# Kernel optimization log

Hardware: AMD Instinct MI355X
Metric: run time of the kernel (lower is better)

The kernel has to match this reference:

```python
import jax, jax.numpy as jnp
import numpy as np

NEG_SLOPE = 0.2


def gat_conv(x, src, dst, n, W, a_src, a_dst, b):
    # x: [N, Din], W: [Din, Dout], a_src/a_dst: [Dout], b: [Dout]
    h = x @ W                                   # [N, Dout]
    alpha_src = h @ a_src                       # [N] score contribution of source nodes
    alpha_dst = h @ a_dst                       # [N]
    e = jax.nn.leaky_relu(alpha_src[src] + alpha_dst[dst], NEG_SLOPE)  # [E]
    # segment softmax over destination nodes (every node has a self-loop -> no empty segs)
    m = jax.ops.segment_max(e, dst, num_segments=n)
    p = jnp.exp(e - m[dst])
    denom = jax.ops.segment_sum(p, dst, num_segments=n)
    coeff = p / denom[dst]                      # [E]
    out = jax.ops.segment_sum(h[src] * coeff[:, None], dst, num_segments=n)
    return out + b


def setup_inputs() -> dict:
    key = jax.random.key(0)
    ks = jax.random.split(key, 16)
    N, E, D_IN, D_H, C = 50000, 800000, 256, 256, 10
    x = jax.random.normal(ks[0], (N, D_IN), dtype=jnp.float32)
    edge_index = jax.random.randint(ks[1], (2, E), 0, N, dtype=jnp.int64)
    s = 0.1
    params = {
        "W1": jax.random.normal(ks[2], (D_IN, D_H), jnp.float32) * s,
        "a_src1": jax.random.normal(ks[3], (D_H,), jnp.float32) * s,
        "a_dst1": jax.random.normal(ks[4], (D_H,), jnp.float32) * s,
        "b1": jnp.zeros((D_H,), jnp.float32),
        "W2": jax.random.normal(ks[5], (D_H, D_H), jnp.float32) * s,
        "a_src2": jax.random.normal(ks[6], (D_H,), jnp.float32) * s,
        "a_dst2": jax.random.normal(ks[7], (D_H,), jnp.float32) * s,
        "b2": jnp.zeros((D_H,), jnp.float32),
        "W3": jax.random.normal(ks[8], (D_H, C), jnp.float32) * s,
        "a_src3": jax.random.normal(ks[9], (C,), jnp.float32) * s,
        "a_dst3": jax.random.normal(ks[10], (C,), jnp.float32) * s,
        "b3": jnp.zeros((C,), jnp.float32),
    }
    return {"x": x, "edge_index": edge_index, **params}


def reference(x, edge_index, W1, a_src1, a_dst1, b1, W2, a_src2, a_dst2, b2,
              W3, a_src3, a_dst3, b3):
    n = x.shape[0]
    # PyG GATConv default add_self_loops=True
    loops = jnp.arange(n, dtype=edge_index.dtype)
    src = jnp.concatenate([edge_index[0], loops])
    dst = jnp.concatenate([edge_index[1], loops])
    h = gat_conv(x, src, dst, n, W1, a_src1, a_dst1, b1)
    h = jax.nn.relu(h)
    h = gat_conv(h, src, dst, n, W2, a_src2, a_dst2, b2)
    h = jax.nn.relu(h)
    out = gat_conv(h, src, dst, n, W3, a_src3, a_dst3, b3)
    return out
```

## Files before the change

kernel.cpp:

```cpp
#include <hip/hip_runtime.h>
#include <math.h>

#define N_NODES 50000
#define N_EDGES 800000
#define EP (N_EDGES + N_NODES)
#define NEG_SLOPE 0.2f
#define SCAN_BLOCKS ((N_NODES + 255) / 256)

typedef short short8 __attribute__((ext_vector_type(8)));
typedef float float4_ __attribute__((ext_vector_type(4)));

__device__ __forceinline__ unsigned short f2bf(float f) {
  unsigned int u = __float_as_uint(f);
  u = (u + 0x7FFFu + ((u >> 16) & 1u)) >> 16;
  return (unsigned short)u;
}
__device__ __forceinline__ float bf2f(unsigned int us) {
  return __uint_as_float(us << 16);
}
__device__ __forceinline__ unsigned int pack2(float lo, float hi) {
  return (unsigned int)f2bf(lo) | ((unsigned int)f2bf(hi) << 16);
}

__device__ __forceinline__ int permc(int p) {
  return ((p & 0xE) << 4) | ((p & 1) << 4) | (p >> 4);
}


template <int PERM>
__global__ void cvt_wf_kernel(const float* __restrict__ W, unsigned short* __restrict__ Wf) {
  int t = blockIdx.x * 256 + threadIdx.x;
  int f = t >> 6, lane = t & 63;
  int nt = f >> 3, k0t = f & 7;
  int lm = lane & 15, kg = lane >> 4;
  int kbase = k0t * 32 + kg * 8;
  int n = nt * 16 + lm;
  short8 v;
#pragma unroll
  for (int j = 0; j < 8; ++j) {
    int k = PERM ? permc(kbase + j) : (kbase + j);
    v[j] = (short)f2bf(W[(size_t)k * 256 + n]);
  }
  ((short8*)Wf)[t] = v;
}

__global__ void cvt_wf3_kernel(const float* __restrict__ W3, unsigned short* __restrict__ Wf3) {
  int t = blockIdx.x * 256 + threadIdx.x;
  int k0t = t >> 6, lane = t & 63;
  int lm = lane & 15, kg = lane >> 4;
  int kbase = k0t * 32 + kg * 8;
  short8 v;
#pragma unroll
  for (int j = 0; j < 8; ++j) {
    int k = permc(kbase + j);
    v[j] = (lm < 10) ? (short)f2bf(W3[(size_t)k * 10 + lm]) : (short)0;
  }
  ((short8*)Wf3)[t] = v;
}

__global__ void permute_bias_kernel(const float* __restrict__ b1, const float* __restrict__ b2,
                                    float* __restrict__ pb1, float* __restrict__ pb2) {
  int p = threadIdx.x;
  int c = permc(p);
  pb1[p] = b1[c];
  pb2[p] = b2[c];
}


__global__ void count_kernel(const int* __restrict__ ei, int* __restrict__ cnt) {
  int e = blockIdx.x * 256 + threadIdx.x;
  if (e >= EP) return;
  int dst = (e < N_EDGES) ? ei[N_EDGES + e] : (e - N_EDGES);
  atomicAdd(&cnt[dst], 1);
}

__global__ void scan1_kernel(const int* __restrict__ cnt, int* __restrict__ off,
                             int* __restrict__ bsum) {
  int i = blockIdx.x * 256 + threadIdx.x;
  int v = (i < N_NODES) ? cnt[i] : 0;
  int lane = threadIdx.x & 63, w = threadIdx.x >> 6;
  int x = v;
  for (int o = 1; o < 64; o <<= 1) { int y = __shfl_up(x, o); if (lane >= o) x += y; }
  __shared__ int wsum[4];
  if (lane == 63) wsum[w] = x;
  __syncthreads();
  int add = 0;
  for (int k = 0; k < w; ++k) add += wsum[k];
  if (i < N_NODES) off[i] = x - v + add;
  if (threadIdx.x == 255) bsum[blockIdx.x] = add + x;
}

__global__ void scan2_kernel(int* __restrict__ bsum, int* __restrict__ bpre,
                             int* __restrict__ off) {
  int t = threadIdx.x;
  int v = (t < SCAN_BLOCKS) ? bsum[t] : 0;
  int lane = t & 63, w = t >> 6;
  int x = v;
  for (int o = 1; o < 64; o <<= 1) { int y = __shfl_up(x, o); if (lane >= o) x += y; }
  __shared__ int wsum[4];
  if (lane == 63) wsum[w] = x;
  __syncthreads();
  int add = 0;
  for (int k = 0; k < w; ++k) add += wsum[k];
  if (t < SCAN_BLOCKS) bpre[t] = x - v + add;
  if (t == 255) off[N_NODES] = add + x;
}

__global__ void scan3_kernel(int* __restrict__ off, const int* __restrict__ bpre) {
  int i = blockIdx.x * 256 + threadIdx.x;
  if (i < N_NODES) off[i] += bpre[blockIdx.x];
}

__global__ void scatter_kernel(const int* __restrict__ ei, const int* __restrict__ off,
                               int* __restrict__ cnt, int* __restrict__ esrc) {
  int e = blockIdx.x * 256 + threadIdx.x;
  if (e >= EP) return;
  int src, dst;
  if (e < N_EDGES) { src = ei[e]; dst = ei[N_EDGES + e]; }
  else { src = dst = e - N_EDGES; }
  int pos = off[dst] + atomicAdd(&cnt[dst], 1);
  esrc[pos] = src;
}


template <int AF32>
__global__ __launch_bounds__(512, 2) void gemm_mfma4(const void* __restrict__ Av,
                                                     const uint4* __restrict__ Wf,
                                                     unsigned short* __restrict__ C,
                                                     const float* __restrict__ asrc,
                                                     const float* __restrict__ adst,
                                                     float* __restrict__ as_,
                                                     float* __restrict__ ad_, int M) {
  __shared__ uint4 Bl[8192];
  int tid = threadIdx.x;
#pragma unroll
  for (int i = 0; i < 16; ++i) Bl[i * 512 + tid] = Wf[i * 512 + tid];
  int wave = tid >> 6, lane = tid & 63;
  int lm = lane & 15, kg = lane >> 4;
  int row0 = blockIdx.x * 256 + wave * 32;
  int ar0 = row0 + lm, ar1 = row0 + 16 + lm;
  if (ar0 >= M) ar0 = M - 1;
  if (ar1 >= M) ar1 = M - 1;

  auto loadA = [&](int k0t, int ar) -> short8 {
    if (AF32) {
      const float* A = (const float*)Av;
      const float* p = A + (size_t)ar * 256 + kg * 8 + k0t * 32;
      float4 f0 = *(const float4*)p, f1 = *(const float4*)(p + 4);
      return (short8){(short)f2bf(f0.x), (short)f2bf(f0.y), (short)f2bf(f0.z), (short)f2bf(f0.w),
                      (short)f2bf(f1.x), (short)f2bf(f1.y), (short)f2bf(f1.z), (short)f2bf(f1.w)};
    } else {
      const unsigned short* A = (const unsigned short*)Av;
      return *(const short8*)(A + (size_t)ar * 256 + kg * 8 + k0t * 32);
    }
  };

  float4_ acc0[16], acc1[16];
#pragma unroll
  for (int i = 0; i < 16; ++i) { acc0[i] = (float4_){0, 0, 0, 0}; acc1[i] = (float4_){0, 0, 0, 0}; }
  short8 a0 = loadA(0, ar0), a1 = loadA(0, ar1);
  __syncthreads();
  const short8* Bf = (const short8*)Bl;
  for (int k0t = 0; k0t < 8; ++k0t) {
    short8 na0, na1;
    if (k0t < 7) { na0 = loadA(k0t + 1, ar0); na1 = loadA(k0t + 1, ar1); }
#pragma unroll
    for (int nt = 0; nt < 16; ++nt) {
      short8 b = Bf[(nt * 8 + k0t) * 64 + lane];
      acc0[nt] = __builtin_amdgcn_mfma_f32_16x16x32_bf16(a0, b, acc0[nt], 0, 0, 0);
      acc1[nt] = __builtin_amdgcn_mfma_f32_16x16x32_bf16(a1, b, acc1[nt], 0, 0, 0);
    }
    a0 = na0; a1 = na1;
  }
  float avs[16], avd[16];
#pragma unroll
  for (int nt = 0; nt < 16; ++nt) { avs[nt] = asrc[nt * 16 + lm]; avd[nt] = adst[nt * 16 + lm]; }
#pragma unroll
  for (int g = 0; g < 2; ++g) {
    int rbase = row0 + g * 16 + kg * 4;
#pragma unroll
    for (int i = 0; i < 4; ++i) {
      int r = rbase + i;
      float s = 0.f, dd = 0.f;
      unsigned int u[8];
#pragma unroll
      for (int j = 0; j < 8; ++j) {
        float vlo = g ? acc1[2 * j][i] : acc0[2 * j][i];
        float vhi = g ? acc1[2 * j + 1][i] : acc0[2 * j + 1][i];
        u[j] = pack2(vlo, vhi);
        s += vlo * avs[2 * j] + vhi * avs[2 * j + 1];
        dd += vlo * avd[2 * j] + vhi * avd[2 * j + 1];
      }
      if (r < M) {
        uint4* cp = (uint4*)(C + (size_t)r * 256 + lm * 16);
        cp[0] = (uint4){u[0], u[1], u[2], u[3]};
        cp[1] = (uint4){u[4], u[5], u[6], u[7]};
      }
#pragma unroll
      for (int o = 1; o < 16; o <<= 1) { s += __shfl_xor(s, o); dd += __shfl_xor(dd, o); }
      if (lm == 0 && r < M) { as_[r] = s; ad_[r] = dd; }
    }
  }
}


__global__ __launch_bounds__(256) void gemm_c3_kernel(const unsigned short* __restrict__ X,
                                                      const unsigned short* __restrict__ Wf3,
                                                      const float* __restrict__ asrc,
                                                      const float* __restrict__ adst,
                                                      float* __restrict__ h3p,
                                                      float* __restrict__ as_,
                                                      float* __restrict__ ad_, int M) {
  int tid = threadIdx.x;
  int wave = tid >> 6, lane = tid & 63;
  int lm = lane & 15, kg = lane >> 4;
  int row0 = blockIdx.x * 128 + wave * 32;
  int ar0 = row0 + lm, ar1 = row0 + 16 + lm;
  if (ar0 >= M) ar0 = M - 1;
  if (ar1 >= M) ar1 = M - 1;
  short8 bf[8];
#pragma unroll
  for (int k0t = 0; k0t < 8; ++k0t) bf[k0t] = ((const short8*)Wf3)[k0t * 64 + lane];
  float4_ acc0 = (float4_){0, 0, 0, 0}, acc1 = (float4_){0, 0, 0, 0};
#pragma unroll
  for (int k0t = 0; k0t < 8; ++k0t) {
    int k0 = k0t * 32;
    short8 a0 = *(const short8*)(X + (size_t)ar0 * 256 + kg * 8 + k0);
    short8 a1 = *(const short8*)(X + (size_t)ar1 * 256 + kg * 8 + k0);
    acc0 = __builtin_amdgcn_mfma_f32_16x16x32_bf16(a0, bf[k0t], acc0, 0, 0, 0);
    acc1 = __builtin_amdgcn_mfma_f32_16x16x32_bf16(a1, bf[k0t], acc1, 0, 0, 0);
  }
  float avs = (lm < 10) ? asrc[lm] : 0.f;
  float avd = (lm < 10) ? adst[lm] : 0.f;
#pragma unroll
  for (int g = 0; g < 2; ++g) {
    int rbase = row0 + g * 16 + kg * 4;
#pragma unroll
    for (int i = 0; i < 4; ++i) {
      int r = rbase + i;
      float v = g ? acc1[i] : acc0[i];
      if (r < M) h3p[(size_t)r * 16 + lm] = v;
      float s = v * avs, dd = v * avd;
#pragma unroll
      for (int o = 1; o < 16; o <<= 1) { s += __shfl_xor(s, o); dd += __shfl_xor(dd, o); }
      if (lm == 0 && r < M) { as_[r] = s; ad_[r] = dd; }
    }
  }
}


__global__ __launch_bounds__(256) void agg_fused_kernel(const int* __restrict__ off,
                                                        const int* __restrict__ esrc,
                                                        const float* __restrict__ as_,
                                                        const float* __restrict__ ad_,
                                                        const unsigned short* __restrict__ h,
                                                        const float* __restrict__ pbias,
                                                        unsigned short* __restrict__ outg) {
  __shared__ int s_src[4][64];
  __shared__ float s_p[4][64];
  int wave = threadIdx.x >> 6, lane = threadIdx.x & 63;
  int pair = lane >> 5, cl = lane & 31;
  int d = blockIdx.x * 4 + wave;
  int s0 = off[d], s1 = off[d + 1];
  float adv = ad_[d];
  const uint4* hp4 = (const uint4*)h;
  float a0 = 0.f, a1 = 0.f, a2 = 0.f, a3 = 0.f, a4 = 0.f, a5 = 0.f, a6 = 0.f, a7 = 0.f;
  float sum = 0.f;
  for (int base = s0; base < s1; base += 64) {
    int m = s1 - base; if (m > 64) m = 64;
    int sv = 0; float p = 0.f;
    if (lane < m) {
      sv = esrc[base + lane];
      float e = as_[sv] + adv;
      e = e > 0.f ? e : NEG_SLOPE * e;
      p = __expf(e);
    }
    s_src[wave][lane] = sv;
    s_p[wave][lane] = p;
    float ps = p;
    for (int o = 32; o; o >>= 1) ps += __shfl_xor(ps, o);
    sum += ps;
    int nb = (m + 1) >> 1;
    int j = 0;
    for (; j + 8 <= nb; j += 8) {
#pragma unroll
      for (int u = 0; u < 8; ++u) {
        int idx = (j + u) * 2 + pair;
        int src = s_src[wave][idx];
        float w = s_p[wave][idx];
        uint4 pv = hp4[(size_t)src * 32 + cl];
        a0 = fmaf(w, bf2f(pv.x & 0xffffu), a0); a1 = fmaf(w, bf2f(pv.x >> 16), a1);
        a2 = fmaf(w, bf2f(pv.y & 0xffffu), a2); a3 = fmaf(w, bf2f(pv.y >> 16), a3);
        a4 = fmaf(w, bf2f(pv.z & 0xffffu), a4); a5 = fmaf(w, bf2f(pv.z >> 16), a5);
        a6 = fmaf(w, bf2f(pv.w & 0xffffu), a6); a7 = fmaf(w, bf2f(pv.w >> 16), a7);
      }
    }
    for (; j < nb; ++j) {
      int idx = j * 2 + pair;
      int src = s_src[wave][idx];
      float w = s_p[wave][idx];
      uint4 pv = hp4[(size_t)src * 32 + cl];
      a0 = fmaf(w, bf2f(pv.x & 0xffffu), a0); a1 = fmaf(w, bf2f(pv.x >> 16), a1);
      a2 = fmaf(w, bf2f(pv.y & 0xffffu), a2); a3 = fmaf(w, bf2f(pv.y >> 16), a3);
      a4 = fmaf(w, bf2f(pv.z & 0xffffu), a4); a5 = fmaf(w, bf2f(pv.z >> 16), a5);
      a6 = fmaf(w, bf2f(pv.w & 0xffffu), a6); a7 = fmaf(w, bf2f(pv.w >> 16), a7);
    }
  }
  a0 += __shfl_xor(a0, 32); a1 += __shfl_xor(a1, 32);
  a2 += __shfl_xor(a2, 32); a3 += __shfl_xor(a3, 32);
  a4 += __shfl_xor(a4, 32); a5 += __shfl_xor(a5, 32);
  a6 += __shfl_xor(a6, 32); a7 += __shfl_xor(a7, 32);
  if (pair == 0) {
    float inv = 1.0f / sum;
    float4 b0 = ((const float4*)pbias)[2 * cl];
    float4 b1 = ((const float4*)pbias)[2 * cl + 1];
    float o0 = fmaxf(fmaf(a0, inv, b0.x), 0.f);
    float o1 = fmaxf(fmaf(a1, inv, b0.y), 0.f);
    float o2 = fmaxf(fmaf(a2, inv, b0.z), 0.f);
    float o3 = fmaxf(fmaf(a3, inv, b0.w), 0.f);
    float o4 = fmaxf(fmaf(a4, inv, b1.x), 0.f);
    float o5 = fmaxf(fmaf(a5, inv, b1.y), 0.f);
    float o6 = fmaxf(fmaf(a6, inv, b1.z), 0.f);
    float o7 = fmaxf(fmaf(a7, inv, b1.w), 0.f);
    uint4 ov = (uint4){pack2(o0, o1), pack2(o2, o3), pack2(o4, o5), pack2(o6, o7)};
    ((uint4*)outg)[(size_t)d * 32 + cl] = ov;
  }
}


__global__ __launch_bounds__(256) void agg10_fused_kernel(const int* __restrict__ off,
                                                          const int* __restrict__ esrc,
                                                          const float* __restrict__ as_,
                                                          const float* __restrict__ ad_,
                                                          const float* __restrict__ h3p,
                                                          const float* __restrict__ bias,
                                                          float* __restrict__ out) {
  __shared__ int s_src[4][64];
  __shared__ float s_p[4][64];
  int wave = threadIdx.x >> 6, lane = threadIdx.x & 63;
  int d = blockIdx.x * 4 + wave;
  if (d >= N_NODES) return;
  int s0 = off[d], s1 = off[d + 1];
  float adv = ad_[d];
  int er = lane >> 2;
  int part = lane & 3;
  float ax = 0.f, ay = 0.f, az = 0.f, aw = 0.f;
  float sum = 0.f;
  const float4* hp = (const float4*)h3p;
  for (int base = s0; base < s1; base += 64) {
    int m = s1 - base; if (m > 64) m = 64;
    int sv = 0; float p = 0.f;
    if (lane < m) {
      sv = esrc[base + lane];
      float e = as_[sv] + adv;
      e = e > 0.f ? e : NEG_SLOPE * e;
      p = __expf(e);
    }
    s_src[wave][lane] = sv;
    s_p[wave][lane] = p;
    float ps = p;
    for (int o = 32; o; o >>= 1) ps += __shfl_xor(ps, o);
    sum += ps;
    int ng = (m + 15) >> 4;
    for (int g = 0; g < ng; ++g) {
      int idx = g * 16 + er;
      int src = s_src[wave][idx];
      float w = s_p[wave][idx];
      float4 v = hp[(size_t)src * 4 + part];
      ax = fmaf(w, v.x, ax); ay = fmaf(w, v.y, ay);
      az = fmaf(w, v.z, az); aw = fmaf(w, v.w, aw);
    }
  }
  for (int o = 4; o < 64; o <<= 1) {
    ax += __shfl_xor(ax, o); ay += __shfl_xor(ay, o);
    az += __shfl_xor(az, o); aw += __shfl_xor(aw, o);
  }
  if (lane < 3) {
    float inv = 1.0f / sum;
    float* op = out + (size_t)d * 10 + 4 * lane;
    float2 lo = {fmaf(ax, inv, bias[4 * lane]), fmaf(ay, inv, bias[4 * lane + 1])};
    *(float2*)op = lo;
    if (lane < 2) {
      float2 hi = {fmaf(az, inv, bias[4 * lane + 2]), fmaf(aw, inv, bias[4 * lane + 3])};
      *(float2*)(op + 2) = hi;
    }
  }
}


extern "C" void kernel_launch(void* const* d_in, const int* in_sizes, int n_in,
                              void* d_out, int out_size, void* d_ws, size_t ws_size,
                              hipStream_t stream) {
  const float* x   = (const float*)d_in[0];
  const int*   ei  = (const int*)d_in[1];
  const float* W1  = (const float*)d_in[2];
  const float* as1 = (const float*)d_in[3];
  const float* ad1 = (const float*)d_in[4];
  const float* b1  = (const float*)d_in[5];
  const float* W2  = (const float*)d_in[6];
  const float* as2 = (const float*)d_in[7];
  const float* ad2 = (const float*)d_in[8];
  const float* b2  = (const float*)d_in[9];
  const float* W3  = (const float*)d_in[10];
  const float* as3 = (const float*)d_in[11];
  const float* ad3 = (const float*)d_in[12];
  const float* b3  = (const float*)d_in[13];
  float* out = (float*)d_out;

  char* ws = (char*)d_ws;
  size_t off_b = 0;
  auto alloc = [&](size_t bytes) -> char* {
    char* p = ws + off_b;
    off_b += (bytes + 255) & ~(size_t)255;
    return p;
  };
  unsigned short* hb   = (unsigned short*)alloc((size_t)N_NODES * 256 * 2);
  unsigned short* gb   = (unsigned short*)alloc((size_t)N_NODES * 256 * 2);
  unsigned short* Wf1  = (unsigned short*)alloc(256 * 256 * 2);
  unsigned short* Wf2  = (unsigned short*)alloc(256 * 256 * 2);
  unsigned short* Wf3  = (unsigned short*)alloc(8 * 64 * 8 * 2);
  float* pb1   = (float*)alloc(256 * 4);
  float* pb2   = (float*)alloc(256 * 4);
  float* h3p   = (float*)alloc((size_t)N_NODES * 16 * 4);
  float* as_   = (float*)alloc((size_t)N_NODES * 4);
  float* ad_   = (float*)alloc((size_t)N_NODES * 4);
  int*   roff  = (int*)alloc((size_t)(N_NODES + 1) * 4);
  int*   cnt   = (int*)alloc((size_t)N_NODES * 4);
  int*   bsum  = (int*)alloc((size_t)SCAN_BLOCKS * 4);
  int*   bpre  = (int*)alloc((size_t)SCAN_BLOCKS * 4);
  int*   esrc  = (int*)alloc((size_t)EP * 4);

  cvt_wf_kernel<0><<<32, 256, 0, stream>>>(W1, Wf1);
  cvt_wf_kernel<1><<<32, 256, 0, stream>>>(W2, Wf2);
  cvt_wf3_kernel<<<2, 256, 0, stream>>>(W3, Wf3);
  permute_bias_kernel<<<1, 256, 0, stream>>>(b1, b2, pb1, pb2);

  hipMemsetAsync(cnt, 0, N_NODES * 4, stream);
  int eb = (EP + 255) / 256;
  count_kernel<<<eb, 256, 0, stream>>>(ei, cnt);
  scan1_kernel<<<SCAN_BLOCKS, 256, 0, stream>>>(cnt, roff, bsum);
  scan2_kernel<<<1, 256, 0, stream>>>(bsum, bpre, roff);
  scan3_kernel<<<SCAN_BLOCKS, 256, 0, stream>>>(roff, bpre);
  hipMemsetAsync(cnt, 0, N_NODES * 4, stream);
  scatter_kernel<<<eb, 256, 0, stream>>>(ei, roff, cnt, esrc);

  int g4blocks = (N_NODES + 255) / 256;
  int g3blocks = (N_NODES + 127) / 128;
  int ablocks = (N_NODES + 3) / 4;

  gemm_mfma4<1><<<g4blocks, 512, 0, stream>>>(x, (const uint4*)Wf1, hb, as1, ad1, as_, ad_, N_NODES);
  agg_fused_kernel<<<ablocks, 256, 0, stream>>>(roff, esrc, as_, ad_, hb, pb1, gb);
  gemm_mfma4<0><<<g4blocks, 512, 0, stream>>>(gb, (const uint4*)Wf2, hb, as2, ad2, as_, ad_, N_NODES);
  agg_fused_kernel<<<ablocks, 256, 0, stream>>>(roff, esrc, as_, ad_, hb, pb2, gb);
  gemm_c3_kernel<<<g3blocks, 256, 0, stream>>>(gb, Wf3, as3, ad3, h3p, as_, ad_, N_NODES);
  agg10_fused_kernel<<<ablocks, 256, 0, stream>>>(roff, esrc, as_, ad_, h3p, b3, out);
}
```

Baseline: 411.5 us.

## Merge setup kernels, reuse count buffer in scatter, retile GEMM to 384 threads

The three weight-conversion kernels and the bias-permute kernel become one setup launch. The scatter pass now counts down from the degree counts with atomicSub, so the second memset is no longer needed. The GEMM goes from 512 threads (256 rows per block) to 384 threads (192 rows per block) with launch bounds of one block per CU, and it drops software prefetch of the A tile. The aggregation inner unroll is cut from 8 to 4. Together these cut launch overhead but may reduce latency hiding in the GEMM and aggregation loops.

```diff
diff --git a/kernel.cpp b/kernel.cpp
--- a/kernel.cpp
+++ b/kernel.cpp
@@ -27,43 +27,48 @@
 }
 
 
-template <int PERM>
-__global__ void cvt_wf_kernel(const float* __restrict__ W, unsigned short* __restrict__ Wf) {
-  int t = blockIdx.x * 256 + threadIdx.x;
-  int f = t >> 6, lane = t & 63;
-  int nt = f >> 3, k0t = f & 7;
-  int lm = lane & 15, kg = lane >> 4;
-  int kbase = k0t * 32 + kg * 8;
-  int n = nt * 16 + lm;
-  short8 v;
-#pragma unroll
-  for (int j = 0; j < 8; ++j) {
-    int k = PERM ? permc(kbase + j) : (kbase + j);
-    v[j] = (short)f2bf(W[(size_t)k * 256 + n]);
-  }
-  ((short8*)Wf)[t] = v;
-}
-
-__global__ void cvt_wf3_kernel(const float* __restrict__ W3, unsigned short* __restrict__ Wf3) {
-  int t = blockIdx.x * 256 + threadIdx.x;
-  int k0t = t >> 6, lane = t & 63;
-  int lm = lane & 15, kg = lane >> 4;
-  int kbase = k0t * 32 + kg * 8;
-  short8 v;
-#pragma unroll
-  for (int j = 0; j < 8; ++j) {
-    int k = permc(kbase + j);
-    v[j] = (lm < 10) ? (short)f2bf(W3[(size_t)k * 10 + lm]) : (short)0;
-  }
-  ((short8*)Wf3)[t] = v;
-}
-
-__global__ void permute_bias_kernel(const float* __restrict__ b1, const float* __restrict__ b2,
-                                    float* __restrict__ pb1, float* __restrict__ pb2) {
-  int p = threadIdx.x;
-  int c = permc(p);
-  pb1[p] = b1[c];
-  pb2[p] = b2[c];
+__global__ void setup_kernel(const float* __restrict__ W1, const float* __restrict__ W2,
+                             const float* __restrict__ W3, const float* __restrict__ b1,
+                             const float* __restrict__ b2,
+                             unsigned short* __restrict__ Wf1, unsigned short* __restrict__ Wf2,
+                             unsigned short* __restrict__ Wf3,
+                             float* __restrict__ pb1, float* __restrict__ pb2) {
+  int blk = blockIdx.x;
+  int tid = threadIdx.x;
+  if (blk < 64) {
+    int perm = blk >= 32;
+    const float* W = perm ? W2 : W1;
+    unsigned short* Wf = perm ? Wf2 : Wf1;
+    int t = (blk & 31) * 256 + tid;
+    int f = t >> 6, lane = t & 63;
+    int nt = f >> 3, k0t = f & 7;
+    int lm = lane & 15, kg = lane >> 4;
+    int kbase = k0t * 32 + kg * 8;
+    int n = nt * 16 + lm;
+    short8 v;
+#pragma unroll
+    for (int j = 0; j < 8; ++j) {
+      int k = perm ? permc(kbase + j) : (kbase + j);
+      v[j] = (short)f2bf(W[(size_t)k * 256 + n]);
+    }
+    ((short8*)Wf)[t] = v;
+  } else if (blk < 66) {
+    int t = (blk - 64) * 256 + tid;
+    int k0t = t >> 6, lane = t & 63;
+    int lm = lane & 15, kg = lane >> 4;
+    int kbase = k0t * 32 + kg * 8;
+    short8 v;
+#pragma unroll
+    for (int j = 0; j < 8; ++j) {
+      int k = permc(kbase + j);
+      v[j] = (lm < 10) ? (short)f2bf(W3[(size_t)k * 10 + lm]) : (short)0;
+    }
+    ((short8*)Wf3)[t] = v;
+  } else {
+    int c = permc(tid);
+    pb1[tid] = b1[c];
+    pb2[tid] = b2[c];
+  }
 }
 
 
@@ -118,13 +123,13 @@
   int src, dst;
   if (e < N_EDGES) { src = ei[e]; dst = ei[N_EDGES + e]; }
   else { src = dst = e - N_EDGES; }
-  int pos = off[dst] + atomicAdd(&cnt[dst], 1);
+  int pos = off[dst] + atomicSub(&cnt[dst], 1) - 1;
   esrc[pos] = src;
 }
 
 
 template <int AF32>
-__global__ __launch_bounds__(512, 2) void gemm_mfma4(const void* __restrict__ Av,
+__global__ __launch_bounds__(384, 1) void gemm_mfma4(const void* __restrict__ Av,
                                                      const uint4* __restrict__ Wf,
                                                      unsigned short* __restrict__ C,
                                                      const float* __restrict__ asrc,
@@ -133,44 +138,42 @@
                                                      float* __restrict__ ad_, int M) {
   __shared__ uint4 Bl[8192];
   int tid = threadIdx.x;
-#pragma unroll
-  for (int i = 0; i < 16; ++i) Bl[i * 512 + tid] = Wf[i * 512 + tid];
+  for (int i = tid; i < 8192; i += 384) Bl[i] = Wf[i];
   int wave = tid >> 6, lane = tid & 63;
   int lm = lane & 15, kg = lane >> 4;
-  int row0 = blockIdx.x * 256 + wave * 32;
+  int row0 = blockIdx.x * 192 + wave * 32;
   int ar0 = row0 + lm, ar1 = row0 + 16 + lm;
   if (ar0 >= M) ar0 = M - 1;
   if (ar1 >= M) ar1 = M - 1;
-
-  auto loadA = [&](int k0t, int ar) -> short8 {
-    if (AF32) {
-      const float* A = (const float*)Av;
-      const float* p = A + (size_t)ar * 256 + kg * 8 + k0t * 32;
-      float4 f0 = *(const float4*)p, f1 = *(const float4*)(p + 4);
-      return (short8){(short)f2bf(f0.x), (short)f2bf(f0.y), (short)f2bf(f0.z), (short)f2bf(f0.w),
-                      (short)f2bf(f1.x), (short)f2bf(f1.y), (short)f2bf(f1.z), (short)f2bf(f1.w)};
-    } else {
-      const unsigned short* A = (const unsigned short*)Av;
-      return *(const short8*)(A + (size_t)ar * 256 + kg * 8 + k0t * 32);
-    }
-  };
-
   float4_ acc0[16], acc1[16];
 #pragma unroll
   for (int i = 0; i < 16; ++i) { acc0[i] = (float4_){0, 0, 0, 0}; acc1[i] = (float4_){0, 0, 0, 0}; }
-  short8 a0 = loadA(0, ar0), a1 = loadA(0, ar1);
   __syncthreads();
   const short8* Bf = (const short8*)Bl;
   for (int k0t = 0; k0t < 8; ++k0t) {
-    short8 na0, na1;
-    if (k0t < 7) { na0 = loadA(k0t + 1, ar0); na1 = loadA(k0t + 1, ar1); }
+    int k0 = k0t * 32;
+    short8 a0, a1;
+    if (AF32) {
+      const float* A = (const float*)Av;
+      const float* p0 = A + (size_t)ar0 * 256 + kg * 8 + k0;
+      const float* p1 = A + (size_t)ar1 * 256 + kg * 8 + k0;
+      float4 f0 = *(const float4*)p0, f1 = *(const float4*)(p0 + 4);
+      float4 g0 = *(const float4*)p1, g1 = *(const float4*)(p1 + 4);
+      a0 = (short8){(short)f2bf(f0.x), (short)f2bf(f0.y), (short)f2bf(f0.z), (short)f2bf(f0.w),
+                    (short)f2bf(f1.x), (short)f2bf(f1.y), (short)f2bf(f1.z), (short)f2bf(f1.w)};
+      a1 = (short8){(short)f2bf(g0.x), (short)f2bf(g0.y), (short)f2bf(g0.z), (short)f2bf(g0.w),
+                    (short)f2bf(g1.x), (short)f2bf(g1.y), (short)f2bf(g1.z), (short)f2bf(g1.w)};
+    } else {
+      const unsigned short* A = (const unsigned short*)Av;
+      a0 = *(const short8*)(A + (size_t)ar0 * 256 + kg * 8 + k0);
+      a1 = *(const short8*)(A + (size_t)ar1 * 256 + kg * 8 + k0);
+    }
 #pragma unroll
     for (int nt = 0; nt < 16; ++nt) {
       short8 b = Bf[(nt * 8 + k0t) * 64 + lane];
       acc0[nt] = __builtin_amdgcn_mfma_f32_16x16x32_bf16(a0, b, acc0[nt], 0, 0, 0);
       acc1[nt] = __builtin_amdgcn_mfma_f32_16x16x32_bf16(a1, b, acc1[nt], 0, 0, 0);
     }
-    a0 = na0; a1 = na1;
   }
   float avs[16], avd[16];
 #pragma unroll
@@ -282,9 +285,9 @@
     sum += ps;
     int nb = (m + 1) >> 1;
     int j = 0;
-    for (; j + 8 <= nb; j += 8) {
-#pragma unroll
-      for (int u = 0; u < 8; ++u) {
+    for (; j + 4 <= nb; j += 4) {
+#pragma unroll
+      for (int u = 0; u < 4; ++u) {
         int idx = (j + u) * 2 + pair;
         int src = s_src[wave][idx];
         float w = s_p[wave][idx];
@@ -430,10 +433,7 @@
   int*   bpre  = (int*)alloc((size_t)SCAN_BLOCKS * 4);
   int*   esrc  = (int*)alloc((size_t)EP * 4);
 
-  cvt_wf_kernel<0><<<32, 256, 0, stream>>>(W1, Wf1);
-  cvt_wf_kernel<1><<<32, 256, 0, stream>>>(W2, Wf2);
-  cvt_wf3_kernel<<<2, 256, 0, stream>>>(W3, Wf3);
-  permute_bias_kernel<<<1, 256, 0, stream>>>(b1, b2, pb1, pb2);
+  setup_kernel<<<67, 256, 0, stream>>>(W1, W2, W3, b1, b2, Wf1, Wf2, Wf3, pb1, pb2);
 
   hipMemsetAsync(cnt, 0, N_NODES * 4, stream);
   int eb = (EP + 255) / 256;
@@ -441,16 +441,15 @@
   scan1_kernel<<<SCAN_BLOCKS, 256, 0, stream>>>(cnt, roff, bsum);
   scan2_kernel<<<1, 256, 0, stream>>>(bsum, bpre, roff);
   scan3_kernel<<<SCAN_BLOCKS, 256, 0, stream>>>(roff, bpre);
-  hipMemsetAsync(cnt, 0, N_NODES * 4, stream);
   scatter_kernel<<<eb, 256, 0, stream>>>(ei, roff, cnt, esrc);
 
-  int g4blocks = (N_NODES + 255) / 256;
+  int g4blocks = (N_NODES + 191) / 192;
   int g3blocks = (N_NODES + 127) / 128;
   int ablocks = (N_NODES + 3) / 4;
 
-  gemm_mfma4<1><<<g4blocks, 512, 0, stream>>>(x, (const uint4*)Wf1, hb, as1, ad1, as_, ad_, N_NODES);
+  gemm_mfma4<1><<<g4blocks, 384, 0, stream>>>(x, (const uint4*)Wf1, hb, as1, ad1, as_, ad_, N_NODES);
   agg_fused_kernel<<<ablocks, 256, 0, stream>>>(roff, esrc, as_, ad_, hb, pb1, gb);
-  gemm_mfma4<0><<<g4blocks, 512, 0, stream>>>(gb, (const uint4*)Wf2, hb, as2, ad2, as_, ad_, N_NODES);
+  gemm_mfma4<0><<<g4blocks, 384, 0, stream>>>(gb, (const uint4*)Wf2, hb, as2, ad2, as_, ad_, N_NODES);
   agg_fused_kernel<<<ablocks, 256, 0, stream>>>(roff, esrc, as_, ad_, hb, pb2, gb);
   gemm_c3_kernel<<<g3blocks, 256, 0, stream>>>(gb, Wf3, as3, ad3, h3p, as_, ad_, N_NODES);
   agg10_fused_kernel<<<ablocks, 256, 0, stream>>>(roff, esrc, as_, ad_, h3p, b3, out);
```

Result: no change. 415.9 us (+1.1%).
